# Kernel tuning notes

Measured on AMD Instinct MI355X. Metric: run time of the kernel, lower is better.

## Reference

```python
import jax, jax.numpy as jnp
from jax import lax
import numpy as np

CLIP = 20.0  # DeepSpeech clipped-ReLU bound


def setup_inputs() -> dict:
    key = jax.random.key(0)
    k1, k2, k3 = jax.random.split(key, 3)
    B, T, F, U_ = 32, 800, 161, 1024
    inputs = jax.random.normal(k1, (B, T, F), dtype=jnp.float32)
    W = jax.random.normal(k2, (F, U_), dtype=jnp.float32) * 0.05
    U = jax.random.normal(k3, (U_, U_), dtype=jnp.float32) * 0.02
    b = jnp.zeros((U_,), dtype=jnp.float32)
    return {"inputs": inputs, "W": W, "U": U, "b": b}


def reference(inputs, W, U, b):
    # inputs: [B, T, F]; shared cell weights for both directions.
    B = inputs.shape[0]
    units = U.shape[0]
    # Precompute input projection for all timesteps: [T, B, units]
    xW = (jnp.einsum('btf,fu->btu', inputs, W) + b).transpose(1, 0, 2)
    h0 = jnp.zeros((B, units), dtype=inputs.dtype)

    def step(h, x):
        h = jnp.minimum(jax.nn.relu(x + h @ U), CLIP)
        return h, None

    hf, _ = lax.scan(step, h0, xW)                 # final state, forward direction
    hb, _ = lax.scan(step, h0, xW, reverse=True)   # final state, go_backwards
    return hf + hb
```

## Files before the change

kernel.cpp:

```cpp
#include <hip/hip_runtime.h>
#include <hip/hip_bf16.h>

#define T_STEPS 800
#define BATCH   32
#define FEAT    161
#define UNITS   1024
#define CLIPV   20.0f

typedef __attribute__((ext_vector_type(8))) short short8;
typedef __attribute__((ext_vector_type(4))) float f32x4;
typedef unsigned short u16;
typedef unsigned int   u32;
typedef unsigned long long u64;

__device__ __forceinline__ float bf16_f(u16 u) {
    return __uint_as_float(((u32)u) << 16);
}
__device__ __forceinline__ u16 bf16_rn(float x) {
    __hip_bfloat16 b = __float2bfloat16(x);
    return *(u16*)&b;
}
__device__ __forceinline__ u64 ld_agent_u64(const u64* p) {
    return __hip_atomic_load(p, __ATOMIC_RELAXED, __HIP_MEMORY_SCOPE_AGENT);
}
__device__ __forceinline__ float ld_agent_f(const float* p) {
    return __hip_atomic_load(p, __ATOMIC_RELAXED, __HIP_MEMORY_SCOPE_AGENT);
}
__device__ __forceinline__ void st_agent_f(float* p, float v) {
    __hip_atomic_store(p, v, __ATOMIC_RELAXED, __HIP_MEMORY_SCOPE_AGENT);
}
__device__ __forceinline__ void st_agent_u32(u32* p, u32 v) {
    __hip_atomic_store(p, v, __ATOMIC_RELAXED, __HIP_MEMORY_SCOPE_AGENT);
}
__device__ __forceinline__ short8 ld_agent_b16x8(const u16* p) {
    union { u64 q[2]; short8 v; } u;
    u.q[0] = ld_agent_u64((const u64*)p);
    u.q[1] = ld_agent_u64((const u64*)p + 1);
    return u.v;
}

__global__ __launch_bounds__(256) void init_ws(float* hbuf, u32* flags) {
    int gid = blockIdx.x * 256 + threadIdx.x;
    for (int i = gid; i < 2 * 64 * UNITS; i += 64 * 256) hbuf[i] = 0.f;
    if (gid < 256) flags[gid] = 0u;
}

__global__ __launch_bounds__(256) void u_split_t(const float* __restrict__ U,
                                                 u16* __restrict__ Ut1,
                                                 u16* __restrict__ Ut2,
                                                 u16* __restrict__ Ut3) {
    __shared__ float tile[32][33];
    int bx = blockIdx.x, by = blockIdx.y;
    int lx = threadIdx.x & 31;
    int ly4 = (threadIdx.x >> 5) * 4;
    #pragma unroll
    for (int j = 0; j < 4; ++j)
        tile[ly4 + j][lx] = U[(size_t)(by * 32 + ly4 + j) * UNITS + bx * 32 + lx];
    __syncthreads();
    #pragma unroll
    for (int j = 0; j < 4; ++j) {
        float x = tile[lx][ly4 + j];
        size_t o = (size_t)(bx * 32 + ly4 + j) * UNITS + by * 32 + lx;
        u16 s1 = bf16_rn(x);  float r1 = x - bf16_f(s1);
        u16 s2 = bf16_rn(r1); float r2 = r1 - bf16_f(s2);
        u16 s3 = bf16_rn(r2);
        Ut1[o] = s1; Ut2[o] = s2; Ut3[o] = s3;
    }
}

__global__ __launch_bounds__(256) void xw_gemm(const float* __restrict__ inp,
                                               const float* __restrict__ W,
                                               const float* __restrict__ bias,
                                               float* __restrict__ xW) {
    __shared__ float xs[8 * FEAT];
    int t = blockIdx.x;
    int b0 = blockIdx.y * 8;
    int tid = threadIdx.x;

    for (int i = tid; i < 8 * FEAT; i += 256) {
        int j = i / FEAT;
        int f = i - j * FEAT;
        xs[i] = inp[((size_t)(b0 + j) * T_STEPS + t) * FEAT + f];
    }
    __syncthreads();

    float bv[4];
    #pragma unroll
    for (int c = 0; c < 4; ++c) bv[c] = bias[tid + c * 256];

    float acc[8][4];
    #pragma unroll
    for (int j = 0; j < 8; ++j)
        #pragma unroll
        for (int c = 0; c < 4; ++c) acc[j][c] = bv[c];

    for (int f = 0; f < FEAT; ++f) {
        float w0 = W[(size_t)f * UNITS + tid];
        float w1 = W[(size_t)f * UNITS + tid + 256];
        float w2 = W[(size_t)f * UNITS + tid + 512];
        float w3 = W[(size_t)f * UNITS + tid + 768];
        #pragma unroll
        for (int j = 0; j < 8; ++j) {
            float xv = xs[j * FEAT + f];
            acc[j][0] += xv * w0;
            acc[j][1] += xv * w1;
            acc[j][2] += xv * w2;
            acc[j][3] += xv * w3;
        }
    }

    #pragma unroll
    for (int j = 0; j < 8; ++j)
        #pragma unroll
        for (int c = 0; c < 4; ++c)
            xW[((size_t)t * BATCH + b0 + j) * UNITS + tid + c * 256] = acc[j][c];
}

__global__ __launch_bounds__(512) void rnn_scan(
        const float* __restrict__ xW,
        const u16* __restrict__ Ut1, const u16* __restrict__ Ut2,
        const u16* __restrict__ Ut3,
        float* __restrict__ hbuf, u32* __restrict__ flags,
        float* __restrict__ out) {
    __shared__ f32x4 red[14][64];

    const int tid  = threadIdx.x;
    const int bk   = blockIdx.x;
    const int lane = tid & 63;
    const int kq   = tid >> 6;
    const int quad = lane >> 4;
    const int n16  = lane & 15;
    const int rg   = bk & 3;
    const int ug   = bk >> 2;
    const int R0   = rg * 16;
    const int u0   = ug * 32;
    const int dir  = rg >> 1;

    short8 bfr[4][2][3];
    #pragma unroll
    for (int ks = 0; ks < 4; ++ks) {
        const int koff = kq * 128 + ks * 32 + quad * 8;
        #pragma unroll
        for (int nq = 0; nq < 2; ++nq) {
            const size_t ub = (size_t)(u0 + nq * 16 + n16) * UNITS + koff;
            bfr[ks][nq][0] = ld_agent_b16x8(Ut1 + ub);
            bfr[ks][nq][1] = ld_agent_b16x8(Ut2 + ub);
            bfr[ks][nq][2] = ld_agent_b16x8(Ut3 + ub);
        }
    }

    const size_t HS = (size_t)64 * UNITS;
    u32* myflag = flags + rg * 32 + ug;
    const u64* srcflag = (const u64*)(flags + rg * 32 + kq * 4);

    for (int t = 0; t < T_STEPS; ++t) {
        const size_t sb = (size_t)(t & 1) * HS;
        const size_t db = sb ^ HS;

        float xp[2][4];
        if (kq == 0) {
            const int xt = dir ? (T_STEPS - 1 - t) : t;
            #pragma unroll
            for (int nq = 0; nq < 2; ++nq)
                #pragma unroll
                for (int j = 0; j < 4; ++j) {
                    const int b = (R0 + quad * 4 + j) & 31;
                    xp[nq][j] = xW[(size_t)xt * (BATCH * UNITS) +
                                   (size_t)b * UNITS + u0 + nq * 16 + n16];
                }
        }

        const u32 tgt = (u32)t;
        for (;;) {
            u64 qa = ld_agent_u64(srcflag);
            u64 qb = ld_agent_u64(srcflag + 1);
            u32 f0 = (u32)qa, f1 = (u32)(qa >> 32);
            u32 f2 = (u32)qb, f3 = (u32)(qb >> 32);
            if (f0 >= tgt && f1 >= tgt && f2 >= tgt && f3 >= tgt) break;
        }

        f32x4 acc[2][2] = {{{0.f,0.f,0.f,0.f},{0.f,0.f,0.f,0.f}},
                           {{0.f,0.f,0.f,0.f},{0.f,0.f,0.f,0.f}}};
        #pragma unroll
        for (int ks = 0; ks < 4; ++ks) {
            const float* ap = hbuf + sb + (size_t)(R0 + n16) * UNITS +
                              kq * 128 + ks * 32 + quad * 8;
            union { u64 q[4]; float f[8]; u32 u[8]; } hv;
            hv.q[0] = ld_agent_u64((const u64*)ap);
            hv.q[1] = ld_agent_u64((const u64*)ap + 1);
            hv.q[2] = ld_agent_u64((const u64*)ap + 2);
            hv.q[3] = ld_agent_u64((const u64*)ap + 3);
            short8 a1, a2, a3;
            #pragma unroll
            for (int j = 0; j < 8; ++j) {
                float x = hv.f[j];
                u16 s1 = (u16)(hv.u[j] >> 16);
                float r1 = x - bf16_f(s1);
                u16 s2 = (u16)(__float_as_uint(r1) >> 16);
                float r2 = r1 - bf16_f(s2);
                u16 s3 = (u16)(__float_as_uint(r2) >> 16);
                a1[j] = (short)s1; a2[j] = (short)s2; a3[j] = (short)s3;
            }
            #pragma unroll
            for (int nq = 0; nq < 2; ++nq) {
                acc[nq][0] = __builtin_amdgcn_mfma_f32_16x16x32_bf16(a1, bfr[ks][nq][0], acc[nq][0], 0, 0, 0);
                acc[nq][1] = __builtin_amdgcn_mfma_f32_16x16x32_bf16(a2, bfr[ks][nq][0], acc[nq][1], 0, 0, 0);
                acc[nq][0] = __builtin_amdgcn_mfma_f32_16x16x32_bf16(a1, bfr[ks][nq][1], acc[nq][0], 0, 0, 0);
                acc[nq][1] = __builtin_amdgcn_mfma_f32_16x16x32_bf16(a2, bfr[ks][nq][1], acc[nq][1], 0, 0, 0);
                acc[nq][0] = __builtin_amdgcn_mfma_f32_16x16x32_bf16(a1, bfr[ks][nq][2], acc[nq][0], 0, 0, 0);
                acc[nq][1] = __builtin_amdgcn_mfma_f32_16x16x32_bf16(a3, bfr[ks][nq][0], acc[nq][1], 0, 0, 0);
            }
        }
        f32x4 c0 = acc[0][0] + acc[0][1];
        f32x4 c1 = acc[1][0] + acc[1][1];

        if (kq) {
            red[(kq - 1) * 2 + 0][lane] = c0;
            red[(kq - 1) * 2 + 1][lane] = c1;
        }
        __syncthreads();
        if (kq == 0) {
            #pragma unroll
            for (int w = 0; w < 7; ++w) {
                c0 += red[w * 2 + 0][lane];
                c1 += red[w * 2 + 1][lane];
            }
            float* hdst = hbuf + db;
            #pragma unroll
            for (int nq = 0; nq < 2; ++nq)
                #pragma unroll
                for (int j = 0; j < 4; ++j) {
                    float a = (nq ? c1[j] : c0[j]) + xp[nq][j];
                    a = fminf(fmaxf(a, 0.f), CLIPV);
                    st_agent_f(hdst + (size_t)(R0 + quad * 4 + j) * UNITS +
                               u0 + nq * 16 + n16, a);
                }
        }
        __syncthreads();
        if (tid == 0) st_agent_u32(myflag, (u32)(t + 1));
    }

    if (rg < 2) {
        const u32* bwd = flags + (rg + 2) * 32 + ug;
        while (__hip_atomic_load(bwd, __ATOMIC_RELAXED,
                                 __HIP_MEMORY_SCOPE_AGENT) < (u32)T_STEPS) {}
        const int r = tid >> 5, c = tid & 31;
        const int b = R0 + r;
        float hf = ld_agent_f(hbuf + (size_t)b * UNITS + u0 + c);
        float hb = ld_agent_f(hbuf + (size_t)(b + 32) * UNITS + u0 + c);
        out[(size_t)b * UNITS + u0 + c] = hf + hb;
    }
}

extern "C" void kernel_launch(void* const* d_in, const int* in_sizes, int n_in,
                              void* d_out, int out_size, void* d_ws, size_t ws_size,
                              hipStream_t stream) {
    const float* inp  = (const float*)d_in[0];
    const float* W    = (const float*)d_in[1];
    const float* U    = (const float*)d_in[2];
    const float* bias = (const float*)d_in[3];
    float* out = (float*)d_out;

    u16*   Ut1 = (u16*)d_ws;
    u16*   Ut2 = Ut1 + (size_t)UNITS * UNITS;
    u16*   Ut3 = Ut2 + (size_t)UNITS * UNITS;
    float* xW  = (float*)(Ut3 + (size_t)UNITS * UNITS);
    float* hbuf = xW + (size_t)T_STEPS * BATCH * UNITS;
    u32*   flags = (u32*)(hbuf + (size_t)2 * 64 * UNITS);

    init_ws<<<64, 256, 0, stream>>>(hbuf, flags);
    u_split_t<<<dim3(32, 32), 256, 0, stream>>>(U, Ut1, Ut2, Ut3);
    xw_gemm<<<dim3(800, 4), 256, 0, stream>>>(inp, W, bias, xW);

    void* args[] = {(void*)&xW, (void*)&Ut1, (void*)&Ut2, (void*)&Ut3,
                    (void*)&hbuf, (void*)&flags, (void*)&out};
    hipLaunchCooperativeKernel((const void*)rnn_scan, dim3(128), dim3(512),
                               args, 0, stream);
}
```

Before: 4.326 ms.

## Embed step tags in packed bf16-split hidden state to replace flag barriers

Measured after the change: 8.529 ms. 1.97x slower.

```diff
diff --git a/kernel.cpp b/kernel.cpp
--- a/kernel.cpp
+++ b/kernel.cpp
@@ -23,13 +23,7 @@
 __device__ __forceinline__ u64 ld_agent_u64(const u64* p) {
     return __hip_atomic_load(p, __ATOMIC_RELAXED, __HIP_MEMORY_SCOPE_AGENT);
 }
-__device__ __forceinline__ float ld_agent_f(const float* p) {
-    return __hip_atomic_load(p, __ATOMIC_RELAXED, __HIP_MEMORY_SCOPE_AGENT);
-}
-__device__ __forceinline__ void st_agent_f(float* p, float v) {
-    __hip_atomic_store(p, v, __ATOMIC_RELAXED, __HIP_MEMORY_SCOPE_AGENT);
-}
-__device__ __forceinline__ void st_agent_u32(u32* p, u32 v) {
+__device__ __forceinline__ void st_agent_u64(u64* p, u64 v) {
     __hip_atomic_store(p, v, __ATOMIC_RELAXED, __HIP_MEMORY_SCOPE_AGENT);
 }
 __device__ __forceinline__ short8 ld_agent_b16x8(const u16* p) {
@@ -39,10 +33,9 @@
     return u.v;
 }
 
-__global__ __launch_bounds__(256) void init_ws(float* hbuf, u32* flags) {
+__global__ __launch_bounds__(256) void init_ws(u64* hbuf) {
     int gid = blockIdx.x * 256 + threadIdx.x;
-    for (int i = gid; i < 2 * 64 * UNITS; i += 64 * 256) hbuf[i] = 0.f;
-    if (gid < 256) flags[gid] = 0u;
+    for (int i = gid; i < 2 * 64 * UNITS; i += 64 * 256) hbuf[i] = 0ull;
 }
 
 __global__ __launch_bounds__(256) void u_split_t(const float* __restrict__ U,
@@ -120,9 +113,9 @@
         const float* __restrict__ xW,
         const u16* __restrict__ Ut1, const u16* __restrict__ Ut2,
         const u16* __restrict__ Ut3,
-        float* __restrict__ hbuf, u32* __restrict__ flags,
+        u64* __restrict__ hbuf,
         float* __restrict__ out) {
-    __shared__ f32x4 red[14][64];
+    __shared__ f32x4 red[2][8][2][64];
 
     const int tid  = threadIdx.x;
     const int bk   = blockIdx.x;
@@ -136,6 +129,14 @@
     const int u0   = ug * 32;
     const int dir  = rg >> 1;
 
+    const int er  = tid >> 5;
+    const int ec  = tid & 31;
+    const int enq = ec >> 4;
+    const int ele = ((er >> 2) << 4) + (ec & 15);
+    const int eje = er & 3;
+    const int eb  = (R0 + er) & 31;
+    const size_t hoff = (size_t)(R0 + er) * UNITS + (u0 + ec);
+
     short8 bfr[4][2][3];
     #pragma unroll
     for (int ks = 0; ks < 4; ++ks) {
@@ -150,104 +151,93 @@
     }
 
     const size_t HS = (size_t)64 * UNITS;
-    u32* myflag = flags + rg * 32 + ug;
-    const u64* srcflag = (const u64*)(flags + rg * 32 + kq * 4);
 
     for (int t = 0; t < T_STEPS; ++t) {
         const size_t sb = (size_t)(t & 1) * HS;
         const size_t db = sb ^ HS;
-
-        float xp[2][4];
-        if (kq == 0) {
-            const int xt = dir ? (T_STEPS - 1 - t) : t;
+        const int tb = t & 1;
+
+        const int xt = dir ? (T_STEPS - 1 - t) : t;
+        const float xv = xW[(size_t)xt * (BATCH * UNITS) +
+                            (size_t)eb * UNITS + (u0 + ec)];
+
+        const u64* abase = hbuf + sb + (size_t)(R0 + n16) * UNITS + kq * 128;
+        short8 fa1[4], fa2[4], fa3[4];
+        const u32 tgt = (u32)t;
+        u32 fresh = 0;
+        while (fresh != 0xFu) {
             #pragma unroll
-            for (int nq = 0; nq < 2; ++nq)
+            for (int ks = 0; ks < 4; ++ks) {
+                if (fresh & (1u << ks)) continue;
+                const u64* ap = abase + ks * 32 + quad * 8;
+                u64 w[8];
                 #pragma unroll
-                for (int j = 0; j < 4; ++j) {
-                    const int b = (R0 + quad * 4 + j) & 31;
-                    xp[nq][j] = xW[(size_t)xt * (BATCH * UNITS) +
-                                   (size_t)b * UNITS + u0 + nq * 16 + n16];
+                for (int j = 0; j < 8; ++j) w[j] = ld_agent_u64(ap + j);
+                bool ok = true;
+                #pragma unroll
+                for (int j = 0; j < 8; ++j) ok &= ((u32)(w[j] >> 48) == tgt);
+                if (__all((int)ok)) {
+                    short8 a1, a2, a3;
+                    #pragma unroll
+                    for (int j = 0; j < 8; ++j) {
+                        const u32 lo = (u32)w[j];
+                        const u32 hi = (u32)(w[j] >> 32);
+                        a1[j] = (short)(lo & 0xffffu);
+                        a2[j] = (short)(lo >> 16);
+                        a3[j] = (short)(hi & 0xffffu);
+                    }
+                    fa1[ks] = a1; fa2[ks] = a2; fa3[ks] = a3;
+                    fresh |= 1u << ks;
                 }
-        }
-
-        const u32 tgt = (u32)t;
-        for (;;) {
-            u64 qa = ld_agent_u64(srcflag);
-            u64 qb = ld_agent_u64(srcflag + 1);
-            u32 f0 = (u32)qa, f1 = (u32)(qa >> 32);
-            u32 f2 = (u32)qb, f3 = (u32)(qb >> 32);
-            if (f0 >= tgt && f1 >= tgt && f2 >= tgt && f3 >= tgt) break;
+            }
         }
 
         f32x4 acc[2][2] = {{{0.f,0.f,0.f,0.f},{0.f,0.f,0.f,0.f}},
                            {{0.f,0.f,0.f,0.f},{0.f,0.f,0.f,0.f}}};
         #pragma unroll
         for (int ks = 0; ks < 4; ++ks) {
-            const float* ap = hbuf + sb + (size_t)(R0 + n16) * UNITS +
-                              kq * 128 + ks * 32 + quad * 8;
-            union { u64 q[4]; float f[8]; u32 u[8]; } hv;
-            hv.q[0] = ld_agent_u64((const u64*)ap);
-            hv.q[1] = ld_agent_u64((const u64*)ap + 1);
-            hv.q[2] = ld_agent_u64((const u64*)ap + 2);
-            hv.q[3] = ld_agent_u64((const u64*)ap + 3);
-            short8 a1, a2, a3;
-            #pragma unroll
-            for (int j = 0; j < 8; ++j) {
-                float x = hv.f[j];
-                u16 s1 = (u16)(hv.u[j] >> 16);
-                float r1 = x - bf16_f(s1);
-                u16 s2 = (u16)(__float_as_uint(r1) >> 16);
-                float r2 = r1 - bf16_f(s2);
-                u16 s3 = (u16)(__float_as_uint(r2) >> 16);
-                a1[j] = (short)s1; a2[j] = (short)s2; a3[j] = (short)s3;
-            }
             #pragma unroll
             for (int nq = 0; nq < 2; ++nq) {
-                acc[nq][0] = __builtin_amdgcn_mfma_f32_16x16x32_bf16(a1, bfr[ks][nq][0], acc[nq][0], 0, 0, 0);
-                acc[nq][1] = __builtin_amdgcn_mfma_f32_16x16x32_bf16(a2, bfr[ks][nq][0], acc[nq][1], 0, 0, 0);
-                acc[nq][0] = __builtin_amdgcn_mfma_f32_16x16x32_bf16(a1, bfr[ks][nq][1], acc[nq][0], 0, 0, 0);
-                acc[nq][1] = __builtin_amdgcn_mfma_f32_16x16x32_bf16(a2, bfr[ks][nq][1], acc[nq][1], 0, 0, 0);
-                acc[nq][0] = __builtin_amdgcn_mfma_f32_16x16x32_bf16(a1, bfr[ks][nq][2], acc[nq][0], 0, 0, 0);
-                acc[nq][1] = __builtin_amdgcn_mfma_f32_16x16x32_bf16(a3, bfr[ks][nq][0], acc[nq][1], 0, 0, 0);
+                acc[nq][0] = __builtin_amdgcn_mfma_f32_16x16x32_bf16(fa1[ks], bfr[ks][nq][0], acc[nq][0], 0, 0, 0);
+                acc[nq][1] = __builtin_amdgcn_mfma_f32_16x16x32_bf16(fa2[ks], bfr[ks][nq][0], acc[nq][1], 0, 0, 0);
+                acc[nq][0] = __builtin_amdgcn_mfma_f32_16x16x32_bf16(fa1[ks], bfr[ks][nq][1], acc[nq][0], 0, 0, 0);
+                acc[nq][1] = __builtin_amdgcn_mfma_f32_16x16x32_bf16(fa2[ks], bfr[ks][nq][1], acc[nq][1], 0, 0, 0);
+                acc[nq][0] = __builtin_amdgcn_mfma_f32_16x16x32_bf16(fa1[ks], bfr[ks][nq][2], acc[nq][0], 0, 0, 0);
+                acc[nq][1] = __builtin_amdgcn_mfma_f32_16x16x32_bf16(fa3[ks], bfr[ks][nq][0], acc[nq][1], 0, 0, 0);
             }
         }
-        f32x4 c0 = acc[0][0] + acc[0][1];
-        f32x4 c1 = acc[1][0] + acc[1][1];
-
-        if (kq) {
-            red[(kq - 1) * 2 + 0][lane] = c0;
-            red[(kq - 1) * 2 + 1][lane] = c1;
-        }
+
+        red[tb][kq][0][lane] = acc[0][0] + acc[0][1];
+        red[tb][kq][1][lane] = acc[1][0] + acc[1][1];
         __syncthreads();
-        if (kq == 0) {
-            #pragma unroll
-            for (int w = 0; w < 7; ++w) {
-                c0 += red[w * 2 + 0][lane];
-                c1 += red[w * 2 + 1][lane];
-            }
-            float* hdst = hbuf + db;
-            #pragma unroll
-            for (int nq = 0; nq < 2; ++nq)
-                #pragma unroll
-                for (int j = 0; j < 4; ++j) {
-                    float a = (nq ? c1[j] : c0[j]) + xp[nq][j];
-                    a = fminf(fmaxf(a, 0.f), CLIPV);
-                    st_agent_f(hdst + (size_t)(R0 + quad * 4 + j) * UNITS +
-                               u0 + nq * 16 + n16, a);
-                }
-        }
-        __syncthreads();
-        if (tid == 0) st_agent_u32(myflag, (u32)(t + 1));
+
+        float s = xv;
+        #pragma unroll
+        for (int k2 = 0; k2 < 8; ++k2)
+            s += ((const float*)&red[tb][k2][enq][ele])[eje];
+        s = fminf(fmaxf(s, 0.f), CLIPV);
+
+        const u32 xb = __float_as_uint(s);
+        const u16 s1 = (u16)(xb >> 16);
+        const float r1 = s - bf16_f(s1);
+        const u16 s2 = (u16)(__float_as_uint(r1) >> 16);
+        const float r2 = r1 - bf16_f(s2);
+        const u16 s3 = (u16)(__float_as_uint(r2) >> 16);
+        const u64 wv = (u64)s1 | ((u64)s2 << 16) | ((u64)s3 << 32) |
+                       ((u64)(u32)(t + 1) << 48);
+        st_agent_u64(hbuf + db + hoff, wv);
     }
 
     if (rg < 2) {
-        const u32* bwd = flags + (rg + 2) * 32 + ug;
-        while (__hip_atomic_load(bwd, __ATOMIC_RELAXED,
-                                 __HIP_MEMORY_SCOPE_AGENT) < (u32)T_STEPS) {}
         const int r = tid >> 5, c = tid & 31;
         const int b = R0 + r;
-        float hf = ld_agent_f(hbuf + (size_t)b * UNITS + u0 + c);
-        float hb = ld_agent_f(hbuf + (size_t)(b + 32) * UNITS + u0 + c);
+        const u64* pf = hbuf + (size_t)b * UNITS + u0 + c;
+        const u64* pb = hbuf + (size_t)(b + 32) * UNITS + u0 + c;
+        u64 wf, wb;
+        do { wf = ld_agent_u64(pf); } while ((u32)(wf >> 48) != (u32)T_STEPS);
+        do { wb = ld_agent_u64(pb); } while ((u32)(wb >> 48) != (u32)T_STEPS);
+        const float hf = bf16_f((u16)wf) + bf16_f((u16)(wf >> 16)) + bf16_f((u16)(wf >> 32));
+        const float hb = bf16_f((u16)wb) + bf16_f((u16)(wb >> 16)) + bf16_f((u16)(wb >> 32));
         out[(size_t)b * UNITS + u0 + c] = hf + hb;
     }
 }
@@ -265,15 +255,14 @@
     u16*   Ut2 = Ut1 + (size_t)UNITS * UNITS;
     u16*   Ut3 = Ut2 + (size_t)UNITS * UNITS;
     float* xW  = (float*)(Ut3 + (size_t)UNITS * UNITS);
-    float* hbuf = xW + (size_t)T_STEPS * BATCH * UNITS;
-    u32*   flags = (u32*)(hbuf + (size_t)2 * 64 * UNITS);
-
-    init_ws<<<64, 256, 0, stream>>>(hbuf, flags);
+    u64*   hbuf = (u64*)(xW + (size_t)T_STEPS * BATCH * UNITS);
+
+    init_ws<<<64, 256, 0, stream>>>(hbuf);
     u_split_t<<<dim3(32, 32), 256, 0, stream>>>(U, Ut1, Ut2, Ut3);
     xw_gemm<<<dim3(800, 4), 256, 0, stream>>>(inp, W, bias, xW);
 
     void* args[] = {(void*)&xW, (void*)&Ut1, (void*)&Ut2, (void*)&Ut3,
-                    (void*)&hbuf, (void*)&flags, (void*)&out};
+                    (void*)&hbuf, (void*)&out};
     hipLaunchCooperativeKernel((const void*)rnn_scan, dim3(128), dim3(512),
                                args, 0, stream);
 }
```

## Use per-wave flags and triple-buffered state to drop one barrier per step

Applied to the files above, without the earlier changes.

Measured after the change: 12.19 ms. 182% more time.

```diff
diff --git a/kernel.cpp b/kernel.cpp
--- a/kernel.cpp
+++ b/kernel.cpp
@@ -23,13 +23,13 @@
 __device__ __forceinline__ u64 ld_agent_u64(const u64* p) {
     return __hip_atomic_load(p, __ATOMIC_RELAXED, __HIP_MEMORY_SCOPE_AGENT);
 }
+__device__ __forceinline__ u32 ld_agent_u32(const u32* p) {
+    return __hip_atomic_load(p, __ATOMIC_RELAXED, __HIP_MEMORY_SCOPE_AGENT);
+}
 __device__ __forceinline__ float ld_agent_f(const float* p) {
     return __hip_atomic_load(p, __ATOMIC_RELAXED, __HIP_MEMORY_SCOPE_AGENT);
 }
 __device__ __forceinline__ void st_agent_f(float* p, float v) {
-    __hip_atomic_store(p, v, __ATOMIC_RELAXED, __HIP_MEMORY_SCOPE_AGENT);
-}
-__device__ __forceinline__ void st_agent_u32(u32* p, u32 v) {
     __hip_atomic_store(p, v, __ATOMIC_RELAXED, __HIP_MEMORY_SCOPE_AGENT);
 }
 __device__ __forceinline__ short8 ld_agent_b16x8(const u16* p) {
@@ -41,8 +41,8 @@
 
 __global__ __launch_bounds__(256) void init_ws(float* hbuf, u32* flags) {
     int gid = blockIdx.x * 256 + threadIdx.x;
-    for (int i = gid; i < 2 * 64 * UNITS; i += 64 * 256) hbuf[i] = 0.f;
-    if (gid < 256) flags[gid] = 0u;
+    for (int i = gid; i < 3 * 64 * UNITS; i += 64 * 256) hbuf[i] = 0.f;
+    if (gid < 1024) flags[gid] = 0u;
 }
 
 __global__ __launch_bounds__(256) void u_split_t(const float* __restrict__ U,
@@ -122,7 +122,7 @@
         const u16* __restrict__ Ut3,
         float* __restrict__ hbuf, u32* __restrict__ flags,
         float* __restrict__ out) {
-    __shared__ f32x4 red[14][64];
+    __shared__ float redf[2][8][2][64][5];
 
     const int tid  = threadIdx.x;
     const int bk   = blockIdx.x;
@@ -136,6 +136,14 @@
     const int u0   = ug * 32;
     const int dir  = rg >> 1;
 
+    const int er  = tid >> 5;
+    const int ec  = tid & 31;
+    const int enq = ec >> 4;
+    const int ele = ((er >> 2) << 4) + (ec & 15);
+    const int eje = er & 3;
+    const int eb  = (R0 + er) & 31;
+    const size_t hoff = (size_t)(R0 + er) * UNITS + (u0 + ec);
+
     short8 bfr[4][2][3];
     #pragma unroll
     for (int ks = 0; ks < 4; ++ks) {
@@ -150,33 +158,26 @@
     }
 
     const size_t HS = (size_t)64 * UNITS;
-    u32* myflag = flags + rg * 32 + ug;
-    const u64* srcflag = (const u64*)(flags + rg * 32 + kq * 4);
-
+    const u64* wflag = (const u64*)(flags + (rg * 32 + kq * 4) * 8);
+    u32* myflag = flags + ((size_t)(rg * 32 + ug) * 8) + kq;
+    const int fidx = lane & 15;
+
+    int sb3 = 0;
     for (int t = 0; t < T_STEPS; ++t) {
-        const size_t sb = (size_t)(t & 1) * HS;
-        const size_t db = sb ^ HS;
-
-        float xp[2][4];
-        if (kq == 0) {
-            const int xt = dir ? (T_STEPS - 1 - t) : t;
-            #pragma unroll
-            for (int nq = 0; nq < 2; ++nq)
-                #pragma unroll
-                for (int j = 0; j < 4; ++j) {
-                    const int b = (R0 + quad * 4 + j) & 31;
-                    xp[nq][j] = xW[(size_t)xt * (BATCH * UNITS) +
-                                   (size_t)b * UNITS + u0 + nq * 16 + n16];
-                }
-        }
+        const int db3 = (sb3 == 2) ? 0 : sb3 + 1;
+        const size_t sb = (size_t)sb3 * HS;
+        const size_t db = (size_t)db3 * HS;
+        const int tb = t & 1;
+
+        const int xt = dir ? (T_STEPS - 1 - t) : t;
+        const float xv = xW[(size_t)xt * (BATCH * UNITS) +
+                            (size_t)eb * UNITS + (u0 + ec)];
 
         const u32 tgt = (u32)t;
         for (;;) {
-            u64 qa = ld_agent_u64(srcflag);
-            u64 qb = ld_agent_u64(srcflag + 1);
-            u32 f0 = (u32)qa, f1 = (u32)(qa >> 32);
-            u32 f2 = (u32)qb, f3 = (u32)(qb >> 32);
-            if (f0 >= tgt && f1 >= tgt && f2 >= tgt && f3 >= tgt) break;
+            u64 q = ld_agent_u64(wflag + fidx);
+            int ok = ((u32)q >= tgt) && ((u32)(q >> 32) >= tgt);
+            if (__all(ok)) break;
         }
 
         f32x4 acc[2][2] = {{{0.f,0.f,0.f,0.f},{0.f,0.f,0.f,0.f}},
@@ -214,40 +215,43 @@
         f32x4 c0 = acc[0][0] + acc[0][1];
         f32x4 c1 = acc[1][0] + acc[1][1];
 
-        if (kq) {
-            red[(kq - 1) * 2 + 0][lane] = c0;
-            red[(kq - 1) * 2 + 1][lane] = c1;
+        #pragma unroll
+        for (int j = 0; j < 4; ++j) {
+            redf[tb][kq][0][lane][j] = c0[j];
+            redf[tb][kq][1][lane][j] = c1[j];
         }
         __syncthreads();
-        if (kq == 0) {
+
+        float s = 0.f;
+        #pragma unroll
+        for (int k2 = 0; k2 < 8; ++k2)
+            s += redf[tb][k2][enq][ele][eje];
+        s += xv;
+        s = fminf(fmaxf(s, 0.f), CLIPV);
+        st_agent_f(hbuf + db + hoff, s);
+        if ((tid & 63) == 0)
+            __hip_atomic_store(myflag, (u32)(t + 1), __ATOMIC_RELEASE,
+                               __HIP_MEMORY_SCOPE_AGENT);
+        sb3 = db3;
+    }
+
+    if (rg < 2) {
+        const u32* f0 = flags + (rg * 32 + ug) * 8;
+        const u32* f1 = flags + ((rg + 2) * 32 + ug) * 8;
+        for (;;) {
+            int ok = 1;
             #pragma unroll
-            for (int w = 0; w < 7; ++w) {
-                c0 += red[w * 2 + 0][lane];
-                c1 += red[w * 2 + 1][lane];
+            for (int w = 0; w < 8; ++w) {
+                ok &= (ld_agent_u32(f0 + w) >= (u32)T_STEPS);
+                ok &= (ld_agent_u32(f1 + w) >= (u32)T_STEPS);
             }
-            float* hdst = hbuf + db;
-            #pragma unroll
-            for (int nq = 0; nq < 2; ++nq)
-                #pragma unroll
-                for (int j = 0; j < 4; ++j) {
-                    float a = (nq ? c1[j] : c0[j]) + xp[nq][j];
-                    a = fminf(fmaxf(a, 0.f), CLIPV);
-                    st_agent_f(hdst + (size_t)(R0 + quad * 4 + j) * UNITS +
-                               u0 + nq * 16 + n16, a);
-                }
-        }
-        __syncthreads();
-        if (tid == 0) st_agent_u32(myflag, (u32)(t + 1));
-    }
-
-    if (rg < 2) {
-        const u32* bwd = flags + (rg + 2) * 32 + ug;
-        while (__hip_atomic_load(bwd, __ATOMIC_RELAXED,
-                                 __HIP_MEMORY_SCOPE_AGENT) < (u32)T_STEPS) {}
+            if (ok) break;
+        }
+        const float* fin = hbuf + (size_t)(T_STEPS % 3) * HS;
         const int r = tid >> 5, c = tid & 31;
         const int b = R0 + r;
-        float hf = ld_agent_f(hbuf + (size_t)b * UNITS + u0 + c);
-        float hb = ld_agent_f(hbuf + (size_t)(b + 32) * UNITS + u0 + c);
+        float hf = ld_agent_f(fin + (size_t)b * UNITS + u0 + c);
+        float hb = ld_agent_f(fin + (size_t)(b + 32) * UNITS + u0 + c);
         out[(size_t)b * UNITS + u0 + c] = hf + hb;
     }
 }
@@ -266,7 +270,7 @@
     u16*   Ut3 = Ut2 + (size_t)UNITS * UNITS;
     float* xW  = (float*)(Ut3 + (size_t)UNITS * UNITS);
     float* hbuf = xW + (size_t)T_STEPS * BATCH * UNITS;
-    u32*   flags = (u32*)(hbuf + (size_t)2 * 64 * UNITS);
+    u32*   flags = (u32*)(hbuf + (size_t)3 * 64 * UNITS);
 
     init_ws<<<64, 256, 0, stream>>>(hbuf, flags);
     u_split_t<<<dim3(32, 32), 256, 0, stream>>>(U, Ut1, Ut2, Ut3);
```
